# Performance work log

Measured on AMD Instinct MI355X. Metric: run time of the kernel, lower is better.

Reference implementation:

```python
import jax, jax.numpy as jnp
import numpy as np

INPUT_DIM = 1024
HIDDEN_DIM = 1024


def setup_inputs() -> dict:
    key = jax.random.key(0)
    ks = jax.random.split(key, 7)
    s = 1.0 / np.sqrt(INPUT_DIM)
    x = jax.random.normal(ks[0], (4, 2048, INPUT_DIM), dtype=jnp.float32)
    Wq = jax.random.uniform(ks[1], (INPUT_DIM, HIDDEN_DIM), minval=-s, maxval=s, dtype=jnp.float32)
    bq = jax.random.uniform(ks[2], (HIDDEN_DIM,), minval=-s, maxval=s, dtype=jnp.float32)
    Wk = jax.random.uniform(ks[3], (INPUT_DIM, HIDDEN_DIM), minval=-s, maxval=s, dtype=jnp.float32)
    bk = jax.random.uniform(ks[4], (HIDDEN_DIM,), minval=-s, maxval=s, dtype=jnp.float32)
    Wv = jax.random.uniform(ks[5], (INPUT_DIM, HIDDEN_DIM), minval=-s, maxval=s, dtype=jnp.float32)
    bv = jax.random.uniform(ks[6], (HIDDEN_DIM,), minval=-s, maxval=s, dtype=jnp.float32)
    return {"x": x, "Wq": Wq, "bq": bq, "Wk": Wk, "bk": bk, "Wv": Wv, "bv": bv}


def reference(x, Wq, bq, Wk, bk, Wv, bv):
    # Q, K, V: [B, S, H]
    Q = jnp.einsum('bsd,dh->bsh', x, Wq) + bq
    K = jnp.einsum('bsd,dh->bsh', x, Wk) + bk
    V = jnp.einsum('bsd,dh->bsh', x, Wv) + bv
    scale = 1.0 / jnp.sqrt(jnp.array(Q.shape[-1], dtype=Q.dtype))
    scores = jnp.einsum('bqh,bkh->bqk', Q, K) * scale  # [B, S, S]
    attn = jax.nn.softmax(scores, axis=-1)
    return jnp.einsum('bqk,bkh->bqh', attn, V)
```

## Files before the change

### kernel.cpp

```cpp
#include <hip/hip_runtime.h>
#include <hip/hip_bf16.h>
#include <stdint.h>

typedef unsigned short u16;
typedef __attribute__((ext_vector_type(8))) short short8;
typedef __attribute__((ext_vector_type(4))) float floatx4;

#define BATCH 4
#define SEQ   2048
#define DIM   1024

__device__ inline u16 f2bf(float f) {
  union { float f; uint32_t u; } v; v.f = f;
  uint32_t r = v.u + 0x7fffu + ((v.u >> 16) & 1u);
  return (u16)(r >> 16);
}

__device__ inline uint32_t f2bf2(float lo, float hi) {
  __hip_bfloat162 h = __float22bfloat162_rn(float2{lo, hi});
  union { __hip_bfloat162 h; uint32_t u; } v; v.h = h;
  return v.u;
}

__device__ inline void gload_lds16(const u16* g, u16* l) {
  __builtin_amdgcn_global_load_lds((const __attribute__((address_space(1))) uint32_t*)g,
                                   (__attribute__((address_space(3))) uint32_t*)l,
                                   16, 0, 0);
}

__global__ __launch_bounds__(256) void prep(const float* __restrict__ x,
                                            const float* __restrict__ Wq,
                                            const float* __restrict__ Wk,
                                            const float* __restrict__ Wv,
                                            const float* __restrict__ bq,
                                            const float* __restrict__ bk,
                                            const float* __restrict__ bv,
                                            u16* __restrict__ Xb,
                                            u16* __restrict__ Wt,
                                            float* __restrict__ bias,
                                            float* __restrict__ lsum) {
  __shared__ u16 tile[32][33];
  const int bx = blockIdx.x;
  if (bx < 8192) {
    size_t i = ((size_t)bx * 256 + threadIdx.x) * 4;
    float4 v = *(const float4*)(x + i);
    uint2 o;
    o.x = f2bf2(v.x, v.y);
    o.y = f2bf2(v.z, v.w);
    *(uint2*)(Xb + i) = o;
    if (bx < 8) {
      float4 z = {0.f, 0.f, 0.f, 0.f};
      *(float4*)(lsum + (size_t)bx * 1024 + threadIdx.x * 4) = z;
    }
    return;
  }
  const int t = bx - 8192;
  const int tz = t >> 10;
  const int bxx = t & 31;
  const int byy = (t >> 5) & 31;
  const float* W = (tz == 0) ? Wq : (tz == 1) ? Wk : Wv;
  u16* o = Wt + (size_t)tz * (1u << 20);
  if (bxx == 0 && byy == 0) {
    const float* bsrc = (tz == 0) ? bq : (tz == 1) ? bk : bv;
    float4 b4 = *(const float4*)(bsrc + threadIdx.x * 4);
    *(float4*)(bias + tz * 1024 + threadIdx.x * 4) = b4;
  }
  int c0 = bxx * 32, r0 = byy * 32;
  int tx = threadIdx.x & 31, ty = threadIdx.x >> 5;
#pragma unroll
  for (int p = 0; p < 4; ++p)
    tile[p * 8 + ty][tx] = f2bf(W[(size_t)(r0 + p * 8 + ty) * DIM + c0 + tx]);
  __syncthreads();
#pragma unroll
  for (int p = 0; p < 4; ++p)
    o[(size_t)(c0 + p * 8 + ty) * DIM + r0 + tx] = tile[tx][p * 8 + ty];
}

__global__ __launch_bounds__(256, 3)
void qkv_fused(const u16* __restrict__ Xb, const u16* __restrict__ Wt,
               u16* __restrict__ Q, u16* __restrict__ Vt,
               const float* __restrict__ bias) {
  constexpr int K = 1024;
  __shared__ u16 ldsA[128 * 64];
  __shared__ u16 ldsB[128 * 64];
  const int lane = threadIdx.x & 63;
  const int wave = threadIdx.x >> 6;
  const int z = blockIdx.z;

  int mt, nt, N;
  const u16 *Ab, *Bb;
  if (z < 2) {
    mt = blockIdx.x; nt = blockIdx.y; N = 1024;
    Ab = Xb + (size_t)mt * 128 * K;
    Bb = Wt + (size_t)z * (1u << 20) + (size_t)nt * 128 * K;
  } else {
    nt = blockIdx.x; mt = blockIdx.y; N = 8192;
    Ab = Wt + (size_t)2 * (1u << 20) + (size_t)mt * 128 * K;
    Bb = Xb + (size_t)nt * 128 * K;
  }

  const int sr = lane >> 2;
  const int sc = (lane & 3) * 8;
  const u16* gA0 = Ab + (size_t)(wave * 32 + sr) * K + sc;
  const u16* gB0 = Bb + (size_t)(wave * 32 + sr) * K + sc;
  u16* lA0 = ldsA + wave * 1024;
  u16* lB0 = ldsB + wave * 1024;
  constexpr int SL = 4096;

  const int wm = (wave >> 1) * 64;
  const int wn = (wave & 1) * 64;
  const int fr = lane & 15;
  const int fk = (lane >> 4) * 8;
  const u16* la = ldsA + (wm + fr) * 32 + fk;
  const u16* lb = ldsB + (wn + fr) * 32 + fk;

  floatx4 acc[4][4] = {};

  for (int kt = 0; kt < K; kt += 64) {
    __syncthreads();
#pragma unroll
    for (int i = 0; i < 2; ++i) {
      gload_lds16(gA0 + kt + (size_t)(16 * i) * K, lA0 + i * 512);
      gload_lds16(gA0 + kt + 32 + (size_t)(16 * i) * K, lA0 + SL + i * 512);
      gload_lds16(gB0 + kt + (size_t)(16 * i) * K, lB0 + i * 512);
      gload_lds16(gB0 + kt + 32 + (size_t)(16 * i) * K, lB0 + SL + i * 512);
    }
    __syncthreads();
#pragma unroll
    for (int ks = 0; ks < 2; ++ks) {
      short8 a[4], b[4];
#pragma unroll
      for (int i = 0; i < 4; ++i) a[i] = *(const short8*)(la + ks * SL + i * 512);
#pragma unroll
      for (int i = 0; i < 4; ++i) b[i] = *(const short8*)(lb + ks * SL + i * 512);
#pragma unroll
      for (int mi = 0; mi < 4; ++mi)
#pragma unroll
        for (int ni = 0; ni < 4; ++ni)
          acc[mi][ni] = __builtin_amdgcn_mfma_f32_16x16x32_bf16(a[mi], b[ni], acc[mi][ni], 0, 0, 0);
    }
  }

  const int er = (lane >> 4) * 4;
  const int ec = lane & 15;
  const int r0 = mt * 128 + wm;
  const int c0 = nt * 128 + wn;

  if (z < 2) {
    u16* C = Q + (size_t)z * (8u << 20);
    const float* bz = bias + z * 1024;
    const float zs = (z == 0) ? 0.03125f : 1.0f;
#pragma unroll
    for (int mi = 0; mi < 4; ++mi)
#pragma unroll
      for (int ni = 0; ni < 4; ++ni) {
        const int col = c0 + ni * 16 + ec;
        const float bb = bz[col];
        const int row = r0 + mi * 16 + er;
        const uint32_t p0 = f2bf2((acc[mi][ni][0] + bb) * zs, (acc[mi][ni][1] + bb) * zs);
        const uint32_t p1 = f2bf2((acc[mi][ni][2] + bb) * zs, (acc[mi][ni][3] + bb) * zs);
        C[(size_t)(row + 0) * N + col] = (u16)p0;
        C[(size_t)(row + 1) * N + col] = (u16)(p0 >> 16);
        C[(size_t)(row + 2) * N + col] = (u16)p1;
        C[(size_t)(row + 3) * N + col] = (u16)(p1 >> 16);
      }
  } else {
    const float* bz = bias + 2 * 1024;
#pragma unroll
    for (int mi = 0; mi < 4; ++mi) {
      float bb[4];
#pragma unroll
      for (int r = 0; r < 4; ++r) bb[r] = bz[r0 + mi * 16 + er + r];
#pragma unroll
      for (int ni = 0; ni < 4; ++ni) {
        const int col = c0 + ni * 16 + ec;
        const size_t base = (size_t)(col >> 11) * (1u << 21) + (col & 2047);
        const int row = r0 + mi * 16 + er;
        const uint32_t p0 = f2bf2(acc[mi][ni][0] + bb[0], acc[mi][ni][1] + bb[1]);
        const uint32_t p1 = f2bf2(acc[mi][ni][2] + bb[2], acc[mi][ni][3] + bb[3]);
        Vt[base + (size_t)(row + 0) * 2048] = (u16)p0;
        Vt[base + (size_t)(row + 1) * 2048] = (u16)(p0 >> 16);
        Vt[base + (size_t)(row + 2) * 2048] = (u16)p1;
        Vt[base + (size_t)(row + 3) * 2048] = (u16)(p1 >> 16);
      }
    }
  }
}

template <int EPI, int SWIZ, int TM>
__global__ __launch_bounds__(256, (TM == 256) ? 2 : 3)
void gemm_bt(const u16* __restrict__ A, const u16* __restrict__ Bt,
             void* __restrict__ Cv, float* __restrict__ lsum,
             int M, int N, int K, size_t sA, size_t sB, size_t sC) {
  constexpr int MI = TM / 32;
  constexpr int AS = TM / 64;
  __shared__ u16 ldsA[TM * 64];
  __shared__ u16 ldsB[128 * 64];
  const int lane = threadIdx.x & 63;
  const int wave = threadIdx.x >> 6;

  int mt, nt;
  if (SWIZ == 2) {
    const int lin = blockIdx.x;
    const int c = lin & 7, j = lin >> 3;
    mt = 4 * (c >> 1) + (j & 3);
    nt = 4 * (c & 1) + (j >> 2);
  } else {
    const int lin = blockIdx.x;
    const int c = lin & 7, j = lin >> 3;
    mt = 4 * (c & 1) + (j & 3);
    nt = 4 * (c >> 1) + (j >> 2);
  }

  const u16* Ab = A + sA * blockIdx.z + (size_t)mt * TM * K;
  const u16* Bb = Bt + sB * blockIdx.z + (size_t)nt * 128 * K;

  const int sr = lane >> 2;
  const int sc = (lane & 3) * 8;
  const u16* gA0 = Ab + (size_t)(wave * (TM / 4) + sr) * K + sc;
  const u16* gB0 = Bb + (size_t)(wave * 32 + sr) * K + sc;
  u16* lA0 = ldsA + wave * (TM / 4) * 32;
  u16* lB0 = ldsB + wave * 1024;
  constexpr int SLA = TM * 32;
  constexpr int SLB = 4096;

  const int wm = (wave >> 1) * (TM / 2);
  const int wn = (wave & 1) * 64;
  const int fr = lane & 15;
  const int fk = (lane >> 4) * 8;
  const u16* la = ldsA + (wm + fr) * 32 + fk;
  const u16* lb = ldsB + (wn + fr) * 32 + fk;

  floatx4 acc[MI][4] = {};

  for (int kt = 0; kt < K; kt += 64) {
    __syncthreads();
#pragma unroll
    for (int i = 0; i < AS; ++i) {
      gload_lds16(gA0 + kt + (size_t)(16 * i) * K, lA0 + i * 512);
      gload_lds16(gA0 + kt + 32 + (size_t)(16 * i) * K, lA0 + SLA + i * 512);
    }
#pragma unroll
    for (int i = 0; i < 2; ++i) {
      gload_lds16(gB0 + kt + (size_t)(16 * i) * K, lB0 + i * 512);
      gload_lds16(gB0 + kt + 32 + (size_t)(16 * i) * K, lB0 + SLB + i * 512);
    }
    __syncthreads();
#pragma unroll
    for (int ks = 0; ks < 2; ++ks) {
      short8 a[MI], b[4];
#pragma unroll
      for (int i = 0; i < MI; ++i)
        a[i] = *(const short8*)(la + ks * SLA + i * 512);
#pragma unroll
      for (int i = 0; i < 4; ++i)
        b[i] = *(const short8*)(lb + ks * SLB + i * 512);
#pragma unroll
      for (int mi = 0; mi < MI; ++mi)
#pragma unroll
        for (int ni = 0; ni < 4; ++ni)
          acc[mi][ni] = __builtin_amdgcn_mfma_f32_16x16x32_bf16(a[mi], b[ni], acc[mi][ni], 0, 0, 0);
    }
  }

  const int er = (lane >> 4) * 4;
  const int ec = lane & 15;
  const int r0 = mt * TM + wm;
  const int c0 = nt * 128 + wn;

  if (EPI == 1) {
    u16* C = (u16*)Cv + sC * blockIdx.z;
    float* lz = lsum + blockIdx.z * 2048;
#pragma unroll
    for (int mi = 0; mi < MI; ++mi) {
      float rs[4] = {0.f, 0.f, 0.f, 0.f};
#pragma unroll
      for (int ni = 0; ni < 4; ++ni) {
        const int col = c0 + ni * 16 + ec;
        const int row = r0 + mi * 16 + er;
        float e[4];
#pragma unroll
        for (int r = 0; r < 4; ++r) {
          e[r] = exp2f(acc[mi][ni][r] * 1.44269504088896340736f);
          rs[r] += e[r];
        }
        const uint32_t p0 = f2bf2(e[0], e[1]);
        const uint32_t p1 = f2bf2(e[2], e[3]);
        C[(size_t)(row + 0) * N + col] = (u16)p0;
        C[(size_t)(row + 1) * N + col] = (u16)(p0 >> 16);
        C[(size_t)(row + 2) * N + col] = (u16)p1;
        C[(size_t)(row + 3) * N + col] = (u16)(p1 >> 16);
      }
#pragma unroll
      for (int o = 1; o < 16; o <<= 1)
#pragma unroll
        for (int r = 0; r < 4; ++r) rs[r] += __shfl_xor(rs[r], o);
      if ((lane & 15) == 0) {
#pragma unroll
        for (int r = 0; r < 4; ++r)
          atomicAdd(&lz[r0 + mi * 16 + er + r], rs[r]);
      }
    }
  } else {
    float* C = (float*)Cv + sC * blockIdx.z;
    const float* lz = lsum + blockIdx.z * 2048;
#pragma unroll
    for (int mi = 0; mi < MI; ++mi) {
      float inv[4];
#pragma unroll
      for (int r = 0; r < 4; ++r) inv[r] = 1.0f / lz[r0 + mi * 16 + er + r];
#pragma unroll
      for (int ni = 0; ni < 4; ++ni) {
        const int col = c0 + ni * 16 + ec;
#pragma unroll
        for (int r = 0; r < 4; ++r) {
          const int row = r0 + mi * 16 + er + r;
          C[(size_t)row * N + col] = acc[mi][ni][r] * inv[r];
        }
      }
    }
  }
}

extern "C" void kernel_launch(void* const* d_in, const int* in_sizes, int n_in,
                              void* d_out, int out_size, void* d_ws, size_t ws_size,
                              hipStream_t stream) {
  const float* x  = (const float*)d_in[0];
  const float* Wq = (const float*)d_in[1];
  const float* bq = (const float*)d_in[2];
  const float* Wk = (const float*)d_in[3];
  const float* bk = (const float*)d_in[4];
  const float* Wv = (const float*)d_in[5];
  const float* bv = (const float*)d_in[6];
  float* out = (float*)d_out;

  char* ws = (char*)d_ws;
  const size_t MB = 1ull << 20;
  u16* Q    = (u16*)(ws + 0 * MB);
  u16* Kb   = (u16*)(ws + 16 * MB);
  u16* Vt   = (u16*)(ws + 48 * MB);
  u16* Xb   = (u16*)(ws + 64 * MB);
  u16* Wt   = (u16*)(ws + 80 * MB);
  float* bias = (float*)(ws + 86 * MB);
  float* lsum = (float*)(ws + 87 * MB);
  u16* P    = (u16*)(ws + 88 * MB);
  (void)Kb; (void)ws_size; (void)in_sizes; (void)n_in; (void)out_size;

  prep<<<11264, 256, 0, stream>>>(x, Wq, Wk, Wv, bq, bk, bv, Xb, Wt, bias, lsum);
  qkv_fused<<<dim3(64, 8, 3), 256, 0, stream>>>(Xb, Wt, Q, Vt, bias);
  gemm_bt<1, 4, 256><<<dim3(128, 1, 4), 256, 0, stream>>>(
      Q, Kb, P, lsum, 2048, 2048, 1024,
      (size_t)2097152, (size_t)2097152, (size_t)4194304);
  gemm_bt<2, 2, 128><<<dim3(128, 1, 4), 256, 0, stream>>>(
      P, Vt, out, lsum, 2048, 1024, 2048,
      (size_t)4194304, (size_t)2097152, (size_t)2097152);
}
```

Baseline: 233.4 us.

## Rewrite GEMMs with 4-stage LDS pipeline, 512-thread 256x256 tiles, swizzled LDS

Replaces the double-synced single-buffer GEMM loop with a shared multi-stage pipeline that keeps three K-slices of 32 in flight through direct global-to-LDS loads, using explicit vmcnt waits and a single barrier per step. Blocks grow to 512 threads with 256x256 (or 128x256) output tiles, the LDS layout is XOR-swizzled to cut bank conflicts, and MFMA sections run at raised wave priority. All three GEMM stages (QKV projection, score+exp, PV+normalize) are rewritten to use it with new tile-to-block mappings. The larger tiles and deeper buffering raise LDS and register use and halve the block count, which may reduce occupancy and load balance.

```diff
diff --git a/kernel.cpp b/kernel.cpp
--- a/kernel.cpp
+++ b/kernel.cpp
@@ -76,82 +76,114 @@
     o[(size_t)(c0 + p * 8 + ty) * DIM + r0 + tx] = tile[tx][p * 8 + ty];
 }
 
-__global__ __launch_bounds__(256, 3)
+
+template <int TM>
+__device__ inline void stage_tile(const u16* __restrict__ A, const u16* __restrict__ B,
+                                  int K, int kbase, u16* buf, int tid, int kc) {
+  const int wave = tid >> 6;
+  const int r = tid >> 2;
+  const u16* ga = A + (size_t)r * K + kbase + kc;
+  u16* la = buf + wave * 512;
+#pragma unroll
+  for (int i = 0; i < TM / 128; ++i)
+    gload_lds16(ga + (size_t)(i * 128) * K, la + i * 4096);
+  const u16* gb = B + (size_t)r * K + kbase + kc;
+  u16* lb = buf + TM * 32 + wave * 512;
+#pragma unroll
+  for (int i = 0; i < 2; ++i)
+    gload_lds16(gb + (size_t)(i * 128) * K, lb + i * 4096);
+}
+
+template <int TM>
+__device__ inline void gemm_pipe(const u16* __restrict__ Ab, const u16* __restrict__ Bb,
+                                 int K, u16* lds, floatx4 (&acc)[TM / 32][4]) {
+  constexpr int MI = TM / 32;
+  constexpr int BUFSZ = (TM + 256) * 32;
+  const int tid = threadIdx.x;
+  const int lane = tid & 63;
+  const int wave = tid >> 6;
+  const int wm = (wave >> 2) * (TM / 2);
+  const int wn = (wave & 3) * 64;
+  const int fr = lane & 15;
+  const int loff = fr * 32 + ((((lane >> 4) ^ ((fr >> 1) & 3))) << 3);
+  const int kc = ((tid & 3) ^ ((tid >> 3) & 3)) * 8;
+  const int NT = K >> 5;
+
+  stage_tile<TM>(Ab, Bb, K, 0, lds, tid, kc);
+  stage_tile<TM>(Ab, Bb, K, 32, lds + BUFSZ, tid, kc);
+  stage_tile<TM>(Ab, Bb, K, 64, lds + 2 * BUFSZ, tid, kc);
+  if constexpr (TM == 256) asm volatile("s_waitcnt vmcnt(8)" ::: "memory");
+  else                     asm volatile("s_waitcnt vmcnt(6)" ::: "memory");
+  asm volatile("s_barrier" ::: "memory");
+
+  for (int t = 0; t < NT; ++t) {
+    if (t + 3 < NT)
+      stage_tile<TM>(Ab, Bb, K, (t + 3) * 32, lds + ((t + 3) & 3) * BUFSZ, tid, kc);
+    const u16* bA = lds + (t & 3) * BUFSZ;
+    const u16* bB = bA + TM * 32;
+    short8 a[MI], b[4];
+#pragma unroll
+    for (int i = 0; i < MI; ++i) a[i] = *(const short8*)(bA + (wm + i * 16) * 32 + loff);
+#pragma unroll
+    for (int i = 0; i < 4; ++i) b[i] = *(const short8*)(bB + (wn + i * 16) * 32 + loff);
+    __builtin_amdgcn_s_setprio(1);
+#pragma unroll
+    for (int mi = 0; mi < MI; ++mi)
+#pragma unroll
+      for (int ni = 0; ni < 4; ++ni)
+        acc[mi][ni] = __builtin_amdgcn_mfma_f32_16x16x32_bf16(a[mi], b[ni], acc[mi][ni], 0, 0, 0);
+    __builtin_amdgcn_s_setprio(0);
+    asm volatile("s_waitcnt lgkmcnt(0)" ::: "memory");
+    __builtin_amdgcn_sched_barrier(0);
+    if (t + 3 < NT) {
+      if constexpr (TM == 256) asm volatile("s_waitcnt vmcnt(8)" ::: "memory");
+      else                     asm volatile("s_waitcnt vmcnt(6)" ::: "memory");
+    } else if (t + 2 < NT) {
+      if constexpr (TM == 256) asm volatile("s_waitcnt vmcnt(4)" ::: "memory");
+      else                     asm volatile("s_waitcnt vmcnt(3)" ::: "memory");
+    } else if (t + 1 < NT) {
+      asm volatile("s_waitcnt vmcnt(0)" ::: "memory");
+    }
+    asm volatile("s_barrier" ::: "memory");
+  }
+}
+
+__global__ __launch_bounds__(512, 2)
 void qkv_fused(const u16* __restrict__ Xb, const u16* __restrict__ Wt,
                u16* __restrict__ Q, u16* __restrict__ Vt,
                const float* __restrict__ bias) {
+  __shared__ __align__(16) u16 lds[4 * (256 + 256) * 32];
   constexpr int K = 1024;
-  __shared__ u16 ldsA[128 * 64];
-  __shared__ u16 ldsB[128 * 64];
+  const int z = blockIdx.z;
+  const int x = blockIdx.x;
+  int mt, nt;
+  if (z < 2) { mt = (x & 7) * 4 + ((x >> 3) & 3); nt = x >> 5; }
+  else       { nt = (x & 7) * 4 + ((x >> 3) & 3); mt = x >> 5; }
+  const u16* Ab; const u16* Bb;
+  if (z < 2) {
+    Ab = Xb + (size_t)mt * 256 * K;
+    Bb = Wt + (size_t)z * (1u << 20) + (size_t)nt * 256 * K;
+  } else {
+    Ab = Wt + (size_t)2 * (1u << 20) + (size_t)mt * 256 * K;
+    Bb = Xb + (size_t)nt * 256 * K;
+  }
+
+  floatx4 acc[8][4] = {};
+  gemm_pipe<256>(Ab, Bb, K, lds, acc);
+
   const int lane = threadIdx.x & 63;
   const int wave = threadIdx.x >> 6;
-  const int z = blockIdx.z;
-
-  int mt, nt, N;
-  const u16 *Ab, *Bb;
-  if (z < 2) {
-    mt = blockIdx.x; nt = blockIdx.y; N = 1024;
-    Ab = Xb + (size_t)mt * 128 * K;
-    Bb = Wt + (size_t)z * (1u << 20) + (size_t)nt * 128 * K;
-  } else {
-    nt = blockIdx.x; mt = blockIdx.y; N = 8192;
-    Ab = Wt + (size_t)2 * (1u << 20) + (size_t)mt * 128 * K;
-    Bb = Xb + (size_t)nt * 128 * K;
-  }
-
-  const int sr = lane >> 2;
-  const int sc = (lane & 3) * 8;
-  const u16* gA0 = Ab + (size_t)(wave * 32 + sr) * K + sc;
-  const u16* gB0 = Bb + (size_t)(wave * 32 + sr) * K + sc;
-  u16* lA0 = ldsA + wave * 1024;
-  u16* lB0 = ldsB + wave * 1024;
-  constexpr int SL = 4096;
-
-  const int wm = (wave >> 1) * 64;
-  const int wn = (wave & 1) * 64;
-  const int fr = lane & 15;
-  const int fk = (lane >> 4) * 8;
-  const u16* la = ldsA + (wm + fr) * 32 + fk;
-  const u16* lb = ldsB + (wn + fr) * 32 + fk;
-
-  floatx4 acc[4][4] = {};
-
-  for (int kt = 0; kt < K; kt += 64) {
-    __syncthreads();
-#pragma unroll
-    for (int i = 0; i < 2; ++i) {
-      gload_lds16(gA0 + kt + (size_t)(16 * i) * K, lA0 + i * 512);
-      gload_lds16(gA0 + kt + 32 + (size_t)(16 * i) * K, lA0 + SL + i * 512);
-      gload_lds16(gB0 + kt + (size_t)(16 * i) * K, lB0 + i * 512);
-      gload_lds16(gB0 + kt + 32 + (size_t)(16 * i) * K, lB0 + SL + i * 512);
-    }
-    __syncthreads();
-#pragma unroll
-    for (int ks = 0; ks < 2; ++ks) {
-      short8 a[4], b[4];
-#pragma unroll
-      for (int i = 0; i < 4; ++i) a[i] = *(const short8*)(la + ks * SL + i * 512);
-#pragma unroll
-      for (int i = 0; i < 4; ++i) b[i] = *(const short8*)(lb + ks * SL + i * 512);
-#pragma unroll
-      for (int mi = 0; mi < 4; ++mi)
-#pragma unroll
-        for (int ni = 0; ni < 4; ++ni)
-          acc[mi][ni] = __builtin_amdgcn_mfma_f32_16x16x32_bf16(a[mi], b[ni], acc[mi][ni], 0, 0, 0);
-    }
-  }
-
-  const int er = (lane >> 4) * 4;
-  const int ec = lane & 15;
-  const int r0 = mt * 128 + wm;
-  const int c0 = nt * 128 + wn;
+  const int wm = (wave >> 2) * 128, wn = (wave & 3) * 64;
+  const int er = (lane >> 4) * 4, ec = lane & 15;
+  const int r0 = mt * 256 + wm;
+  const int c0 = nt * 256 + wn;
 
   if (z < 2) {
     u16* C = Q + (size_t)z * (8u << 20);
     const float* bz = bias + z * 1024;
     const float zs = (z == 0) ? 0.03125f : 1.0f;
 #pragma unroll
-    for (int mi = 0; mi < 4; ++mi)
+    for (int mi = 0; mi < 8; ++mi)
 #pragma unroll
       for (int ni = 0; ni < 4; ++ni) {
         const int col = c0 + ni * 16 + ec;
@@ -159,15 +191,15 @@
         const int row = r0 + mi * 16 + er;
         const uint32_t p0 = f2bf2((acc[mi][ni][0] + bb) * zs, (acc[mi][ni][1] + bb) * zs);
         const uint32_t p1 = f2bf2((acc[mi][ni][2] + bb) * zs, (acc[mi][ni][3] + bb) * zs);
-        C[(size_t)(row + 0) * N + col] = (u16)p0;
-        C[(size_t)(row + 1) * N + col] = (u16)(p0 >> 16);
-        C[(size_t)(row + 2) * N + col] = (u16)p1;
-        C[(size_t)(row + 3) * N + col] = (u16)(p1 >> 16);
+        C[(size_t)(row + 0) * 1024 + col] = (u16)p0;
+        C[(size_t)(row + 1) * 1024 + col] = (u16)(p0 >> 16);
+        C[(size_t)(row + 2) * 1024 + col] = (u16)p1;
+        C[(size_t)(row + 3) * 1024 + col] = (u16)(p1 >> 16);
       }
   } else {
     const float* bz = bias + 2 * 1024;
 #pragma unroll
-    for (int mi = 0; mi < 4; ++mi) {
+    for (int mi = 0; mi < 8; ++mi) {
       float bb[4];
 #pragma unroll
       for (int r = 0; r < 4; ++r) bb[r] = bz[r0 + mi * 16 + er + r];
@@ -187,137 +219,93 @@
   }
 }
 
-template <int EPI, int SWIZ, int TM>
-__global__ __launch_bounds__(256, (TM == 256) ? 2 : 3)
-void gemm_bt(const u16* __restrict__ A, const u16* __restrict__ Bt,
-             void* __restrict__ Cv, float* __restrict__ lsum,
-             int M, int N, int K, size_t sA, size_t sB, size_t sC) {
-  constexpr int MI = TM / 32;
-  constexpr int AS = TM / 64;
-  __shared__ u16 ldsA[TM * 64];
-  __shared__ u16 ldsB[128 * 64];
+__global__ __launch_bounds__(512, 2)
+void score_exp(const u16* __restrict__ Q, const u16* __restrict__ Kb,
+               u16* __restrict__ P, float* __restrict__ lsum) {
+  __shared__ __align__(16) u16 lds[4 * (256 + 256) * 32];
+  const int z = blockIdx.z, x = blockIdx.x;
+  const int c = x & 7, j = x >> 3;
+  const int mt = 2 * (c & 3) + (j & 1);
+  const int nt = 4 * (c >> 2) + (j >> 1);
+  const u16* Ab = Q + (size_t)z * (2048 * 1024) + (size_t)mt * 256 * 1024;
+  const u16* Bb = Kb + (size_t)z * (2048 * 1024) + (size_t)nt * 256 * 1024;
+
+  floatx4 acc[8][4] = {};
+  gemm_pipe<256>(Ab, Bb, 1024, lds, acc);
+
   const int lane = threadIdx.x & 63;
   const int wave = threadIdx.x >> 6;
-
-  int mt, nt;
-  if (SWIZ == 2) {
-    const int lin = blockIdx.x;
-    const int c = lin & 7, j = lin >> 3;
-    mt = 4 * (c >> 1) + (j & 3);
-    nt = 4 * (c & 1) + (j >> 2);
-  } else {
-    const int lin = blockIdx.x;
-    const int c = lin & 7, j = lin >> 3;
-    mt = 4 * (c & 1) + (j & 3);
-    nt = 4 * (c >> 1) + (j >> 2);
-  }
-
-  const u16* Ab = A + sA * blockIdx.z + (size_t)mt * TM * K;
-  const u16* Bb = Bt + sB * blockIdx.z + (size_t)nt * 128 * K;
-
-  const int sr = lane >> 2;
-  const int sc = (lane & 3) * 8;
-  const u16* gA0 = Ab + (size_t)(wave * (TM / 4) + sr) * K + sc;
-  const u16* gB0 = Bb + (size_t)(wave * 32 + sr) * K + sc;
-  u16* lA0 = ldsA + wave * (TM / 4) * 32;
-  u16* lB0 = ldsB + wave * 1024;
-  constexpr int SLA = TM * 32;
-  constexpr int SLB = 4096;
-
-  const int wm = (wave >> 1) * (TM / 2);
-  const int wn = (wave & 1) * 64;
-  const int fr = lane & 15;
-  const int fk = (lane >> 4) * 8;
-  const u16* la = ldsA + (wm + fr) * 32 + fk;
-  const u16* lb = ldsB + (wn + fr) * 32 + fk;
-
-  floatx4 acc[MI][4] = {};
-
-  for (int kt = 0; kt < K; kt += 64) {
-    __syncthreads();
-#pragma unroll
-    for (int i = 0; i < AS; ++i) {
-      gload_lds16(gA0 + kt + (size_t)(16 * i) * K, lA0 + i * 512);
-      gload_lds16(gA0 + kt + 32 + (size_t)(16 * i) * K, lA0 + SLA + i * 512);
-    }
-#pragma unroll
-    for (int i = 0; i < 2; ++i) {
-      gload_lds16(gB0 + kt + (size_t)(16 * i) * K, lB0 + i * 512);
-      gload_lds16(gB0 + kt + 32 + (size_t)(16 * i) * K, lB0 + SLB + i * 512);
-    }
-    __syncthreads();
-#pragma unroll
-    for (int ks = 0; ks < 2; ++ks) {
-      short8 a[MI], b[4];
-#pragma unroll
-      for (int i = 0; i < MI; ++i)
-        a[i] = *(const short8*)(la + ks * SLA + i * 512);
-#pragma unroll
-      for (int i = 0; i < 4; ++i)
-        b[i] = *(const short8*)(lb + ks * SLB + i * 512);
-#pragma unroll
-      for (int mi = 0; mi < MI; ++mi)
-#pragma unroll
-        for (int ni = 0; ni < 4; ++ni)
-          acc[mi][ni] = __builtin_amdgcn_mfma_f32_16x16x32_bf16(a[mi], b[ni], acc[mi][ni], 0, 0, 0);
-    }
-  }
-
-  const int er = (lane >> 4) * 4;
-  const int ec = lane & 15;
-  const int r0 = mt * TM + wm;
-  const int c0 = nt * 128 + wn;
-
-  if (EPI == 1) {
-    u16* C = (u16*)Cv + sC * blockIdx.z;
-    float* lz = lsum + blockIdx.z * 2048;
-#pragma unroll
-    for (int mi = 0; mi < MI; ++mi) {
-      float rs[4] = {0.f, 0.f, 0.f, 0.f};
-#pragma unroll
-      for (int ni = 0; ni < 4; ++ni) {
-        const int col = c0 + ni * 16 + ec;
-        const int row = r0 + mi * 16 + er;
-        float e[4];
-#pragma unroll
-        for (int r = 0; r < 4; ++r) {
-          e[r] = exp2f(acc[mi][ni][r] * 1.44269504088896340736f);
-          rs[r] += e[r];
-        }
-        const uint32_t p0 = f2bf2(e[0], e[1]);
-        const uint32_t p1 = f2bf2(e[2], e[3]);
-        C[(size_t)(row + 0) * N + col] = (u16)p0;
-        C[(size_t)(row + 1) * N + col] = (u16)(p0 >> 16);
-        C[(size_t)(row + 2) * N + col] = (u16)p1;
-        C[(size_t)(row + 3) * N + col] = (u16)(p1 >> 16);
+  const int wm = (wave >> 2) * 128, wn = (wave & 3) * 64;
+  const int er = (lane >> 4) * 4, ec = lane & 15;
+  const int r0 = mt * 256 + wm;
+  const int c0 = nt * 256 + wn;
+  u16* C = P + (size_t)z * (4u << 20);
+  float* lz = lsum + z * 2048;
+#pragma unroll
+  for (int mi = 0; mi < 8; ++mi) {
+    float rs[4] = {0.f, 0.f, 0.f, 0.f};
+#pragma unroll
+    for (int ni = 0; ni < 4; ++ni) {
+      const int col = c0 + ni * 16 + ec;
+      const int row = r0 + mi * 16 + er;
+      float e[4];
+#pragma unroll
+      for (int r = 0; r < 4; ++r) {
+        e[r] = exp2f(acc[mi][ni][r] * 1.44269504088896340736f);
+        rs[r] += e[r];
       }
-#pragma unroll
-      for (int o = 1; o < 16; o <<= 1)
-#pragma unroll
-        for (int r = 0; r < 4; ++r) rs[r] += __shfl_xor(rs[r], o);
-      if ((lane & 15) == 0) {
-#pragma unroll
-        for (int r = 0; r < 4; ++r)
-          atomicAdd(&lz[r0 + mi * 16 + er + r], rs[r]);
-      }
-    }
-  } else {
-    float* C = (float*)Cv + sC * blockIdx.z;
-    const float* lz = lsum + blockIdx.z * 2048;
-#pragma unroll
-    for (int mi = 0; mi < MI; ++mi) {
-      float inv[4];
-#pragma unroll
-      for (int r = 0; r < 4; ++r) inv[r] = 1.0f / lz[r0 + mi * 16 + er + r];
-#pragma unroll
-      for (int ni = 0; ni < 4; ++ni) {
-        const int col = c0 + ni * 16 + ec;
-#pragma unroll
-        for (int r = 0; r < 4; ++r) {
-          const int row = r0 + mi * 16 + er + r;
-          C[(size_t)row * N + col] = acc[mi][ni][r] * inv[r];
-        }
-      }
+      const uint32_t p0 = f2bf2(e[0], e[1]);
+      const uint32_t p1 = f2bf2(e[2], e[3]);
+      C[(size_t)(row + 0) * 2048 + col] = (u16)p0;
+      C[(size_t)(row + 1) * 2048 + col] = (u16)(p0 >> 16);
+      C[(size_t)(row + 2) * 2048 + col] = (u16)p1;
+      C[(size_t)(row + 3) * 2048 + col] = (u16)(p1 >> 16);
+    }
+#pragma unroll
+    for (int o = 1; o < 16; o <<= 1)
+#pragma unroll
+      for (int r = 0; r < 4; ++r) rs[r] += __shfl_xor(rs[r], o);
+    if ((lane & 15) == 0) {
+#pragma unroll
+      for (int r = 0; r < 4; ++r)
+        atomicAdd(&lz[r0 + mi * 16 + er + r], rs[r]);
+    }
+  }
+}
+
+__global__ __launch_bounds__(512, 2)
+void pv_out(const u16* __restrict__ P, const u16* __restrict__ Vt,
+            float* __restrict__ out, const float* __restrict__ lsum) {
+  __shared__ __align__(16) u16 lds[4 * (128 + 256) * 32];
+  const int z = blockIdx.z, x = blockIdx.x;
+  const int c = x & 7, j = x >> 3;
+  const int mt = 4 * (c >> 1) + (j & 3);
+  const int nt = 2 * (c & 1) + (j >> 2);
+  const u16* Ab = P + (size_t)z * (4u << 20) + (size_t)mt * 128 * 2048;
+  const u16* Bb = Vt + (size_t)z * (2u << 20) + (size_t)nt * 256 * 2048;
+
+  floatx4 acc[4][4] = {};
+  gemm_pipe<128>(Ab, Bb, 2048, lds, acc);
+
+  const int lane = threadIdx.x & 63;
+  const int wave = threadIdx.x >> 6;
+  const int wm = (wave >> 2) * 64, wn = (wave & 3) * 64;
+  const int er = (lane >> 4) * 4, ec = lane & 15;
+  const int r0 = mt * 128 + wm;
+  const int c0 = nt * 256 + wn;
+  float* C = out + (size_t)z * (2048 * 1024);
+  const float* lz = lsum + z * 2048;
+#pragma unroll
+  for (int mi = 0; mi < 4; ++mi) {
+    float inv[4];
+#pragma unroll
+    for (int r = 0; r < 4; ++r) inv[r] = 1.0f / lz[r0 + mi * 16 + er + r];
+#pragma unroll
+    for (int ni = 0; ni < 4; ++ni) {
+      const int col = c0 + ni * 16 + ec;
+#pragma unroll
+      for (int r = 0; r < 4; ++r)
+        C[(size_t)(r0 + mi * 16 + er + r) * 1024 + col] = acc[mi][ni][r] * inv[r];
     }
   }
 }
@@ -344,14 +332,10 @@
   float* bias = (float*)(ws + 86 * MB);
   float* lsum = (float*)(ws + 87 * MB);
   u16* P    = (u16*)(ws + 88 * MB);
-  (void)Kb; (void)ws_size; (void)in_sizes; (void)n_in; (void)out_size;
+  (void)ws_size; (void)in_sizes; (void)n_in; (void)out_size;
 
   prep<<<11264, 256, 0, stream>>>(x, Wq, Wk, Wv, bq, bk, bv, Xb, Wt, bias, lsum);
-  qkv_fused<<<dim3(64, 8, 3), 256, 0, stream>>>(Xb, Wt, Q, Vt, bias);
-  gemm_bt<1, 4, 256><<<dim3(128, 1, 4), 256, 0, stream>>>(
-      Q, Kb, P, lsum, 2048, 2048, 1024,
-      (size_t)2097152, (size_t)2097152, (size_t)4194304);
-  gemm_bt<2, 2, 128><<<dim3(128, 1, 4), 256, 0, stream>>>(
-      P, Vt, out, lsum, 2048, 1024, 2048,
-      (size_t)4194304, (size_t)2097152, (size_t)2097152);
-}
+  qkv_fused<<<dim3(128, 1, 3), 512, 0, stream>>>(Xb, Wt, Q, Vt, bias);
+  score_exp<<<dim3(64, 1, 4), 512, 0, stream>>>(Q, Kb, P, lsum);
+  pv_out<<<dim3(64, 1, 4), 512, 0, stream>>>(P, Vt, out, lsum);
+}
```

After: 243.0 us. 1.04x slower.
